# Optimization experiments

Hardware: AMD Instinct MI355X
Metric: run time of the kernel (lower is better)

Reference implementation:

```python
import jax, jax.numpy as jnp
import numpy as np

B, M = 4, 4096          # events x points-per-event (row_splits are uniform)
N = B * M
IN_DIM, SPACE, PROP, K = 128, 4, 64, 32


def setup_inputs() -> dict:
    key = jax.random.key(0)
    k1, k2, k3, k4, k5 = jax.random.split(key, 5)
    x = jax.random.normal(k1, (N, IN_DIM), jnp.float32)
    row_splits = (jnp.arange(B + 1, dtype=jnp.int32) * M)
    s = 1.0 / np.sqrt(IN_DIM)
    Ws = jax.random.uniform(k2, (IN_DIM, SPACE), jnp.float32, -s, s)
    bs = jax.random.uniform(k3, (SPACE,), jnp.float32, -s, s)
    Wp = jax.random.uniform(k4, (IN_DIM, PROP), jnp.float32, -s, s)
    bp = jax.random.uniform(k5, (PROP,), jnp.float32, -s, s)
    return {"x": x, "Ws": Ws, "bs": bs, "Wp": Wp, "bp": bp, "row_splits": row_splits}


def _gravnet(x, Ws, bs, Wp, bp):
    space = x @ Ws + bs                      # [N, SPACE] learned coordinates
    prop = x @ Wp + bp                       # [N, PROP]  features to propagate
    sp = space.reshape(B, M, SPACE)
    pr = prop.reshape(B, M, PROP)
    # exact KNN within each event (row_splits segment): pairwise squared dists
    sq = jnp.sum(sp * sp, axis=-1)                         # [B, M]
    d2 = sq[:, :, None] + sq[:, None, :] - 2.0 * jnp.einsum("bms,bns->bmn", sp, sp)
    neg_vals, idx = jax.lax.top_k(-d2, K)                  # k smallest dists (incl. self)
    distsq = jnp.maximum(-neg_vals, 0.0)                   # [B, M, K]
    weights = jnp.exp(-10.0 * distsq)                      # [B, M, K]
    gathered = jax.vmap(lambda p, i: p[i])(pr, idx)        # [B, M, K, PROP]
    weighted = gathered * weights[..., None]
    fmean = jnp.mean(weighted, axis=2)                     # [B, M, PROP]
    fmax = jnp.max(weighted, axis=2)                       # [B, M, PROP]
    out = jnp.concatenate([fmean, fmax], axis=-1)          # [B, M, 2*PROP]
    return out.reshape(N, 2 * PROP)


def reference(x, Ws, bs, Wp, bp, row_splits):
    # row_splits encodes uniform segments [0, M, 2M, ...]; KNN never crosses them.
    return _gravnet(x, Ws, bs, Wp, bp)
```

## Files before the change

### kernel.cpp

```cpp
#include <hip/hip_runtime.h>
#include <hip/hip_bf16.h>
#include <math.h>

#define N_TOT   16384
#define M_EV    4096
#define IN_DIM  128
#define SPACE_D 4
#define PROP_D  64
#define K_NN    32
#define CAND_CAP 128
#define MARGIN  0.04f

typedef _Float16 h2 __attribute__((ext_vector_type(2)));
typedef __attribute__((ext_vector_type(8))) _Float16 h16x8;
typedef __attribute__((ext_vector_type(4))) float f32x4;
typedef unsigned long long u64;

__device__ __forceinline__ h2 pkmin(h2 a, h2 b) {
#if __has_builtin(__builtin_elementwise_min)
  return __builtin_elementwise_min(a, b);
#else
  h2 r; r.x = (a.x < b.x) ? a.x : b.x; r.y = (a.y < b.y) ? a.y : b.y; return r;
#endif
}

__device__ __forceinline__ h2 pkrtz(float a, float b) {
  return __builtin_bit_cast(h2, __builtin_amdgcn_cvt_pkrtz(a, b));
}

__device__ __forceinline__ int mbcnt64(u64 mk) {
  return (int)__builtin_amdgcn_mbcnt_hi((unsigned)(mk >> 32),
           __builtin_amdgcn_mbcnt_lo((unsigned)mk, 0u));
}

__global__ __launch_bounds__(256) void linear_kernel(
    const float* __restrict__ x,
    const float* __restrict__ Ws, const float* __restrict__ bs,
    const float* __restrict__ Wp, const float* __restrict__ bp,
    float* __restrict__ space, float* __restrict__ prop)
{
  const int lane = threadIdx.x & 63;
  const int wid  = threadIdx.x >> 6;
  const int r0w  = ((int)blockIdx.x * 4 + wid) * 16;

  __shared__ _Float16 s_wp[PROP_D][IN_DIM + 8];

  for (int e = (int)threadIdx.x; e < IN_DIM * PROP_D; e += 256) {
    const int k = e >> 6, c = e & 63;
    s_wp[c][k] = (_Float16)Wp[e];
  }
  __syncthreads();

  {
    const int r = lane >> 2, c = lane & 3;
    const float4* __restrict__ xq = (const float4*)(x + (size_t)(r0w + r) * IN_DIM);
    float a = bs[c];
    #pragma unroll
    for (int i = 0; i < 32; ++i) {
      const float4 v = xq[i];
      a = fmaf(v.x, Ws[(i * 4 + 0) * SPACE_D + c], a);
      a = fmaf(v.y, Ws[(i * 4 + 1) * SPACE_D + c], a);
      a = fmaf(v.z, Ws[(i * 4 + 2) * SPACE_D + c], a);
      a = fmaf(v.w, Ws[(i * 4 + 3) * SPACE_D + c], a);
    }
    space[(size_t)(r0w + r) * SPACE_D + c] = a;
  }

  f32x4 acc0 = {0.f, 0.f, 0.f, 0.f};
  f32x4 acc1 = {0.f, 0.f, 0.f, 0.f};
  f32x4 acc2 = {0.f, 0.f, 0.f, 0.f};
  f32x4 acc3 = {0.f, 0.f, 0.f, 0.f};

  const int arow = lane & 15;
  const int kgrp = (lane >> 4) * 8;

  #pragma unroll
  for (int kk = 0; kk < 4; ++kk) {
    const float4* xa = (const float4*)(x + (size_t)(r0w + arow) * IN_DIM
                                         + kk * 32 + kgrp);
    const float4 a0 = xa[0], a1 = xa[1];
    uint4 au;
    au.x = __builtin_bit_cast(unsigned, pkrtz(a0.x, a0.y));
    au.y = __builtin_bit_cast(unsigned, pkrtz(a0.z, a0.w));
    au.z = __builtin_bit_cast(unsigned, pkrtz(a1.x, a1.y));
    au.w = __builtin_bit_cast(unsigned, pkrtz(a1.z, a1.w));
    const h16x8 afrag = __builtin_bit_cast(h16x8, au);

    const int kb = kk * 32 + kgrp;
    const h16x8 b0 = *(const h16x8*)&s_wp[ 0 + arow][kb];
    const h16x8 b1 = *(const h16x8*)&s_wp[16 + arow][kb];
    const h16x8 b2 = *(const h16x8*)&s_wp[32 + arow][kb];
    const h16x8 b3 = *(const h16x8*)&s_wp[48 + arow][kb];
    acc0 = __builtin_amdgcn_mfma_f32_16x16x32_f16(afrag, b0, acc0, 0, 0, 0);
    acc1 = __builtin_amdgcn_mfma_f32_16x16x32_f16(afrag, b1, acc1, 0, 0, 0);
    acc2 = __builtin_amdgcn_mfma_f32_16x16x32_f16(afrag, b2, acc2, 0, 0, 0);
    acc3 = __builtin_amdgcn_mfma_f32_16x16x32_f16(afrag, b3, acc3, 0, 0, 0);
  }

  {
    const int rbase = (lane >> 4) * 4;
    const float bp0 = bp[ 0 + arow];
    const float bp1 = bp[16 + arow];
    const float bp2 = bp[32 + arow];
    const float bp3 = bp[48 + arow];
    #pragma unroll
    for (int j = 0; j < 4; ++j) {
      float* pr = prop + (size_t)(r0w + rbase + j) * PROP_D;
      pr[ 0 + arow] = acc0[j] + bp0;
      pr[16 + arow] = acc1[j] + bp1;
      pr[32 + arow] = acc2[j] + bp2;
      pr[48 + arow] = acc3[j] + bp3;
    }
  }
}

__global__ __launch_bounds__(512, 3) void knn_kernel(
    const float4* __restrict__ space,
    const float*  __restrict__ prop,
    float*        __restrict__ out)
{
  const int lane = threadIdx.x & 63;
  const int wid  = threadIdx.x >> 6;
  const int row  = (int)blockIdx.x * 8 + wid;
  const int m0   = row & ~(M_EV - 1);
  const int mloc = row & (M_EV - 1);

  __shared__ uint4 s_pk[M_EV / 2];
  __shared__ int   s_ci[8][CAND_CAP];
  __shared__ uint2 s_w[8][K_NN];
  __shared__ int   s_cnt[8];

  {
    const float4* src = space + m0;
    #pragma unroll
    for (int it = 0; it < 4; ++it) {
      const int i = (int)threadIdx.x + it * 512;
      const float4 a = src[i];
      const float4 b = src[i + 2048];
      s_pk[i] = make_uint4(
        __builtin_bit_cast(unsigned, pkrtz(a.x, b.x)),
        __builtin_bit_cast(unsigned, pkrtz(a.y, b.y)),
        __builtin_bit_cast(unsigned, pkrtz(a.z, b.z)),
        __builtin_bit_cast(unsigned, pkrtz(a.w, b.w)));
    }
  }
  if (lane == 0) s_cnt[wid] = 0;
  __syncthreads();

  const float4 qf = space[m0 + mloc];
  const h2 qx = pkrtz(qf.x, qf.x), qy = pkrtz(qf.y, qf.y);
  const h2 qz = pkrtz(qf.z, qf.z), qw = pkrtz(qf.w, qf.w);

  unsigned pd[32];
  h2 mn; mn.x = (_Float16)65504.f; mn.y = (_Float16)65504.f;
  #pragma unroll
  for (int t = 0; t < 32; ++t) {
    const uint4 u = s_pk[lane + (t << 6)];
    const h2 dx = qx - __builtin_bit_cast(h2, u.x);
    const h2 dy = qy - __builtin_bit_cast(h2, u.y);
    const h2 dz = qz - __builtin_bit_cast(h2, u.z);
    const h2 dw = qw - __builtin_bit_cast(h2, u.w);
    h2 s = dx * dx;
    s = dy * dy + s;
    s = dz * dz + s;
    s = dw * dw + s;
    pd[t] = __builtin_bit_cast(unsigned, s);
    mn = pkmin(mn, s);
  }

  const unsigned mnbits = __builtin_bit_cast(unsigned, mn);
  const unsigned c0 = mnbits & 0xFFFFu, c1 = mnbits >> 16;
  unsigned blo = 0u, bhi = 0x7C00u;
  while (blo < bhi) {
    const unsigned mid = (blo + bhi) >> 1;
    const int c = (int)__popcll(__ballot(c0 <= mid)) +
                  (int)__popcll(__ballot(c1 <= mid));
    if (c >= K_NN) { bhi = mid; if (c == K_NN) break; }
    else blo = mid + 1;
  }
  const float T = (float)__builtin_bit_cast(_Float16, (unsigned short)bhi) + MARGIN;
  const h2 Th = pkrtz(T, T);

  #pragma unroll
  for (int t = 0; t < 32; ++t) {
    const h2 s = __builtin_bit_cast(h2, pd[t]);
    if (s.x <= Th.x) {
      const int pos = atomicAdd(&s_cnt[wid], 1);
      if (pos < CAND_CAP) s_ci[wid][pos] = (t << 6) + lane;
    }
    if (s.y <= Th.y) {
      const int pos = atomicAdd(&s_cnt[wid], 1);
      if (pos < CAND_CAP) s_ci[wid][pos] = (t << 6) + lane + 2048;
    }
  }
  int C = s_cnt[wid];

  if (C > CAND_CAP) {
    const float4* __restrict__ ev = space + m0;
    unsigned lo = 0u, hi = __float_as_uint(T);
    while (lo < hi) {
      const unsigned mid = (lo + hi) >> 1;
      const float fm = __uint_as_float(mid);
      int c = 0;
      #pragma unroll 1
      for (int t = 0; t < 64; ++t) {
        const float4 cc = ev[lane + (t << 6)];
        const float dx = qf.x - cc.x, dy = qf.y - cc.y;
        const float dz = qf.z - cc.z, dw = qf.w - cc.w;
        const float dd = fmaf(dx, dx, fmaf(dy, dy, fmaf(dz, dz, dw * dw)));
        c += (int)__popcll(__ballot(dd <= fm));
      }
      if (c >= K_NN) { hi = mid; if (c == K_NN) break; }
      else lo = mid + 1;
    }
    const float Tf = __uint_as_float(hi);
    int cnt = 0;
    #pragma unroll 1
    for (int pass = 0; pass < 2; ++pass) {
      #pragma unroll 1
      for (int t = 0; t < 64; ++t) {
        const float4 cc = ev[lane + (t << 6)];
        const float dx = qf.x - cc.x, dy = qf.y - cc.y;
        const float dz = qf.z - cc.z, dw = qf.w - cc.w;
        const float dd = fmaf(dx, dx, fmaf(dy, dy, fmaf(dz, dz, dw * dw)));
        const bool p = pass ? (dd == Tf) : (dd < Tf);
        const u64 mk = __ballot(p);
        if (p) {
          const int pos = cnt + mbcnt64(mk);
          if (pos < K_NN) s_ci[wid][pos] = (t << 6) + lane;
        }
        cnt += (int)__popcll(mk);
      }
      if (cnt >= K_NN) break;
    }
    C = K_NN;
  }

  const bool h0 = (lane < C), h1 = (64 + lane < C);
  const int i0 = h0 ? s_ci[wid][lane]      : 0;
  const int i1 = h1 ? s_ci[wid][64 + lane] : 0;
  float v0 = INFINITY, v1 = INFINITY;
  if (h0) {
    const float4 cc = space[m0 + i0];
    const float dx = qf.x - cc.x, dy = qf.y - cc.y;
    const float dz = qf.z - cc.z, dw = qf.w - cc.w;
    v0 = fmaf(dx, dx, fmaf(dy, dy, fmaf(dz, dz, dw * dw)));
  }
  if (h1) {
    const float4 cc = space[m0 + i1];
    const float dx = qf.x - cc.x, dy = qf.y - cc.y;
    const float dz = qf.z - cc.z, dw = qf.w - cc.w;
    v1 = fmaf(dx, dx, fmaf(dy, dy, fmaf(dz, dz, dw * dw)));
  }

  unsigned lo = 0u, hi = __float_as_uint(T);
  while (lo < hi) {
    const unsigned mid = (lo + hi) >> 1;
    const float fm = __uint_as_float(mid);
    const int c = (int)__popcll(__ballot(v0 <= fm)) +
                  (int)__popcll(__ballot(v1 <= fm));
    if (c >= K_NN) { hi = mid; if (c == K_NN) break; }
    else lo = mid + 1;
  }
  const float T2 = __uint_as_float(hi);

  const u64 mkE0 = __ballot(v0 == T2);
  const u64 mkE1 = __ballot(v1 == T2);
  const int L = (int)__popcll(__ballot(v0 < T2)) +
                (int)__popcll(__ballot(v1 < T2));
  const int e = K_NN - L;
  const int nE0 = (int)__popcll(mkE0);
  const bool sel0 = (v0 < T2) || ((v0 == T2) && (mbcnt64(mkE0) < e));
  const bool sel1 = (v1 < T2) || ((v1 == T2) && (nE0 + mbcnt64(mkE1) < e));

  const float w0 = __expf(-10.f * v0);
  const float w1 = __expf(-10.f * v1);

  {
    const u64 mkS0 = __ballot(sel0);
    if (sel0) {
      const int pos = mbcnt64(mkS0);
      s_w[wid][pos] = make_uint2((unsigned)i0, __float_as_uint(w0));
    }
    const int b0 = (int)__popcll(mkS0);
    const u64 mkS1 = __ballot(sel1);
    if (sel1) {
      const int pos = b0 + mbcnt64(mkS1);
      s_w[wid][pos] = make_uint2((unsigned)i1, __float_as_uint(w1));
    }
  }

  float accm = 0.f;
  float accx = -INFINITY;
  const float* __restrict__ pb = prop + ((size_t)m0 << 6) + lane;
  #pragma unroll 8
  for (int n = 0; n < K_NN; ++n) {
    const uint2 wn = s_w[wid][n];
    const float w = __uint_as_float(wn.y);
    const float v = pb[(size_t)wn.x << 6];
    const float wv = w * v;
    accm += wv;
    accx = fmaxf(accx, wv);
  }
  out[(size_t)row * 128 + lane]      = accm * (1.f / K_NN);
  out[(size_t)row * 128 + 64 + lane] = accx;
}

extern "C" void kernel_launch(void* const* d_in, const int* in_sizes, int n_in,
                              void* d_out, int out_size, void* d_ws, size_t ws_size,
                              hipStream_t stream) {
  const float* x  = (const float*)d_in[0];
  const float* Ws = (const float*)d_in[1];
  const float* bs = (const float*)d_in[2];
  const float* Wp = (const float*)d_in[3];
  const float* bp = (const float*)d_in[4];
  float* out = (float*)d_out;

  float* prop  = (float*)d_ws;
  float* space = (float*)((char*)d_ws + (size_t)N_TOT * PROP_D * sizeof(float));

  linear_kernel<<<N_TOT / 64, 256, 0, stream>>>(x, Ws, bs, Wp, bp, space, prop);
  knn_kernel<<<N_TOT / 8, 512, 0, stream>>>((const float4*)space, prop, out);
}
```

Baseline: 52.36 us.

## Precompute packed fp16 coordinates in linear kernel and drop Wp LDS staging

```diff
diff --git a/kernel.cpp b/kernel.cpp
--- a/kernel.cpp
+++ b/kernel.cpp
@@ -37,23 +37,19 @@
     const float* __restrict__ x,
     const float* __restrict__ Ws, const float* __restrict__ bs,
     const float* __restrict__ Wp, const float* __restrict__ bp,
-    float* __restrict__ space, float* __restrict__ prop)
+    float* __restrict__ space, unsigned short* __restrict__ spaceh,
+    float* __restrict__ prop)
 {
   const int lane = threadIdx.x & 63;
   const int wid  = threadIdx.x >> 6;
-  const int r0w  = ((int)blockIdx.x * 4 + wid) * 16;
-
-  __shared__ _Float16 s_wp[PROP_D][IN_DIM + 8];
-
-  for (int e = (int)threadIdx.x; e < IN_DIM * PROP_D; e += 256) {
-    const int k = e >> 6, c = e & 63;
-    s_wp[c][k] = (_Float16)Wp[e];
-  }
-  __syncthreads();
-
-  {
-    const int r = lane >> 2, c = lane & 3;
-    const float4* __restrict__ xq = (const float4*)(x + (size_t)(r0w + r) * IN_DIM);
+  const int r0w  = (int)blockIdx.x * 16;
+  const int arow = lane & 15;
+
+  if ((lane & 15) < 4) {
+    const int r = (wid << 2) + (lane >> 4);
+    const int c = lane & 3;
+    const int gr = r0w + r;
+    const float4* __restrict__ xq = (const float4*)(x + (size_t)gr * IN_DIM);
     float a = bs[c];
     #pragma unroll
     for (int i = 0; i < 32; ++i) {
@@ -63,21 +59,20 @@
       a = fmaf(v.z, Ws[(i * 4 + 2) * SPACE_D + c], a);
       a = fmaf(v.w, Ws[(i * 4 + 3) * SPACE_D + c], a);
     }
-    space[(size_t)(r0w + r) * SPACE_D + c] = a;
-  }
-
-  f32x4 acc0 = {0.f, 0.f, 0.f, 0.f};
-  f32x4 acc1 = {0.f, 0.f, 0.f, 0.f};
-  f32x4 acc2 = {0.f, 0.f, 0.f, 0.f};
-  f32x4 acc3 = {0.f, 0.f, 0.f, 0.f};
-
-  const int arow = lane & 15;
+    space[(size_t)gr * SPACE_D + c] = a;
+    const unsigned short hb =
+        (unsigned short)__builtin_bit_cast(unsigned, pkrtz(a, a));
+    spaceh[((size_t)(gr >> 1) << 3) + (c << 1) + (gr & 1)] = hb;
+  }
+
+  f32x4 acc = {0.f, 0.f, 0.f, 0.f};
   const int kgrp = (lane >> 4) * 8;
+  const int col  = (wid << 4) + arow;
 
   #pragma unroll
   for (int kk = 0; kk < 4; ++kk) {
-    const float4* xa = (const float4*)(x + (size_t)(r0w + arow) * IN_DIM
-                                         + kk * 32 + kgrp);
+    const int kb = kk * 32 + kgrp;
+    const float4* xa = (const float4*)(x + (size_t)(r0w + arow) * IN_DIM + kb);
     const float4 a0 = xa[0], a1 = xa[1];
     uint4 au;
     au.x = __builtin_bit_cast(unsigned, pkrtz(a0.x, a0.y));
@@ -86,36 +81,36 @@
     au.w = __builtin_bit_cast(unsigned, pkrtz(a1.z, a1.w));
     const h16x8 afrag = __builtin_bit_cast(h16x8, au);
 
-    const int kb = kk * 32 + kgrp;
-    const h16x8 b0 = *(const h16x8*)&s_wp[ 0 + arow][kb];
-    const h16x8 b1 = *(const h16x8*)&s_wp[16 + arow][kb];
-    const h16x8 b2 = *(const h16x8*)&s_wp[32 + arow][kb];
-    const h16x8 b3 = *(const h16x8*)&s_wp[48 + arow][kb];
-    acc0 = __builtin_amdgcn_mfma_f32_16x16x32_f16(afrag, b0, acc0, 0, 0, 0);
-    acc1 = __builtin_amdgcn_mfma_f32_16x16x32_f16(afrag, b1, acc1, 0, 0, 0);
-    acc2 = __builtin_amdgcn_mfma_f32_16x16x32_f16(afrag, b2, acc2, 0, 0, 0);
-    acc3 = __builtin_amdgcn_mfma_f32_16x16x32_f16(afrag, b3, acc3, 0, 0, 0);
+    const float w0 = Wp[(kb + 0) * PROP_D + col];
+    const float w1 = Wp[(kb + 1) * PROP_D + col];
+    const float w2 = Wp[(kb + 2) * PROP_D + col];
+    const float w3 = Wp[(kb + 3) * PROP_D + col];
+    const float w4 = Wp[(kb + 4) * PROP_D + col];
+    const float w5 = Wp[(kb + 5) * PROP_D + col];
+    const float w6 = Wp[(kb + 6) * PROP_D + col];
+    const float w7 = Wp[(kb + 7) * PROP_D + col];
+    uint4 bu;
+    bu.x = __builtin_bit_cast(unsigned, pkrtz(w0, w1));
+    bu.y = __builtin_bit_cast(unsigned, pkrtz(w2, w3));
+    bu.z = __builtin_bit_cast(unsigned, pkrtz(w4, w5));
+    bu.w = __builtin_bit_cast(unsigned, pkrtz(w6, w7));
+    const h16x8 bfrag = __builtin_bit_cast(h16x8, bu);
+
+    acc = __builtin_amdgcn_mfma_f32_16x16x32_f16(afrag, bfrag, acc, 0, 0, 0);
   }
 
   {
     const int rbase = (lane >> 4) * 4;
-    const float bp0 = bp[ 0 + arow];
-    const float bp1 = bp[16 + arow];
-    const float bp2 = bp[32 + arow];
-    const float bp3 = bp[48 + arow];
+    const float bpc = bp[col];
     #pragma unroll
-    for (int j = 0; j < 4; ++j) {
-      float* pr = prop + (size_t)(r0w + rbase + j) * PROP_D;
-      pr[ 0 + arow] = acc0[j] + bp0;
-      pr[16 + arow] = acc1[j] + bp1;
-      pr[32 + arow] = acc2[j] + bp2;
-      pr[48 + arow] = acc3[j] + bp3;
-    }
+    for (int j = 0; j < 4; ++j)
+      prop[(size_t)(r0w + rbase + j) * PROP_D + col] = acc[j] + bpc;
   }
 }
 
 __global__ __launch_bounds__(512, 3) void knn_kernel(
     const float4* __restrict__ space,
+    const uint4*  __restrict__ spaceh,
     const float*  __restrict__ prop,
     float*        __restrict__ out)
 {
@@ -131,17 +126,11 @@
   __shared__ int   s_cnt[8];
 
   {
-    const float4* src = space + m0;
+    const uint4* src = spaceh + (size_t)(m0 >> 1);
     #pragma unroll
     for (int it = 0; it < 4; ++it) {
       const int i = (int)threadIdx.x + it * 512;
-      const float4 a = src[i];
-      const float4 b = src[i + 2048];
-      s_pk[i] = make_uint4(
-        __builtin_bit_cast(unsigned, pkrtz(a.x, b.x)),
-        __builtin_bit_cast(unsigned, pkrtz(a.y, b.y)),
-        __builtin_bit_cast(unsigned, pkrtz(a.z, b.z)),
-        __builtin_bit_cast(unsigned, pkrtz(a.w, b.w)));
+      s_pk[i] = src[i];
     }
   }
   if (lane == 0) s_cnt[wid] = 0;
@@ -184,13 +173,14 @@
   #pragma unroll
   for (int t = 0; t < 32; ++t) {
     const h2 s = __builtin_bit_cast(h2, pd[t]);
+    const int p2 = ((t << 6) + lane) << 1;
     if (s.x <= Th.x) {
       const int pos = atomicAdd(&s_cnt[wid], 1);
-      if (pos < CAND_CAP) s_ci[wid][pos] = (t << 6) + lane;
+      if (pos < CAND_CAP) s_ci[wid][pos] = p2;
     }
     if (s.y <= Th.y) {
       const int pos = atomicAdd(&s_cnt[wid], 1);
-      if (pos < CAND_CAP) s_ci[wid][pos] = (t << 6) + lane + 2048;
+      if (pos < CAND_CAP) s_ci[wid][pos] = p2 + 1;
     }
   }
   int C = s_cnt[wid];
@@ -318,7 +308,11 @@
 
   float* prop  = (float*)d_ws;
   float* space = (float*)((char*)d_ws + (size_t)N_TOT * PROP_D * sizeof(float));
-
-  linear_kernel<<<N_TOT / 64, 256, 0, stream>>>(x, Ws, bs, Wp, bp, space, prop);
-  knn_kernel<<<N_TOT / 8, 512, 0, stream>>>((const float4*)space, prop, out);
-}
+  unsigned short* spaceh = (unsigned short*)((char*)space
+                           + (size_t)N_TOT * SPACE_D * sizeof(float));
+
+  linear_kernel<<<N_TOT / 16, 256, 0, stream>>>(x, Ws, bs, Wp, bp,
+                                                space, spaceh, prop);
+  knn_kernel<<<N_TOT / 8, 512, 0, stream>>>((const float4*)space,
+                                            (const uint4*)spaceh, prop, out);
+}
```

After: 51.70 us. No clear change (-1.3%).
